# Kernel optimization log

Hardware: AMD Instinct MI355X
Metric: run time of the kernel (lower is better)

## Reference

```python
import jax, jax.numpy as jnp
import numpy as np

N_NODES = 50000


def gcn_conv(x, edge_index, W, b, n_nodes):
    # PyG GCNConv: add self-loops, symmetric normalization, linear, scatter-add.
    src, dst = edge_index[0], edge_index[1]
    loops = jnp.arange(n_nodes, dtype=src.dtype)
    src = jnp.concatenate([src, loops])
    dst = jnp.concatenate([dst, loops])
    # linear transform first (PyG order), reduces scatter width when out < in
    h = x @ W  # [N, out]
    deg = jax.ops.segment_sum(jnp.ones_like(dst, dtype=h.dtype), dst, num_segments=n_nodes)
    dinv = jnp.where(deg > 0, jax.lax.rsqrt(deg), 0.0)
    norm = dinv[src] * dinv[dst]  # [E+N]
    msgs = h[src] * norm[:, None]  # gather + scale, [E+N, out]
    out = jax.ops.segment_sum(msgs, dst, num_segments=n_nodes)  # scatter-add
    return out + b


def setup_inputs() -> dict:
    key = jax.random.key(0)
    k1, k2, k3, k4 = jax.random.split(key, 4)
    in_c, hid_c, out_c = 256, 128, 64
    n_edges = 800000
    features = jax.random.normal(k1, (N_NODES, in_c), dtype=jnp.float32)
    edge_index = jax.random.randint(k2, (2, n_edges), 0, N_NODES, dtype=jnp.int64)
    W1 = jax.random.normal(k3, (in_c, hid_c), dtype=jnp.float32) * (1.0 / np.sqrt(in_c))
    b1 = jnp.zeros((hid_c,), dtype=jnp.float32)
    W2 = jax.random.normal(k4, (hid_c, out_c), dtype=jnp.float32) * (1.0 / np.sqrt(hid_c))
    b2 = jnp.zeros((out_c,), dtype=jnp.float32)
    return {"features": features, "edge_index": edge_index, "W1": W1, "b1": b1, "W2": W2, "b2": b2}


def reference(features, edge_index, W1, b1, W2, b2):
    n = features.shape[0]
    x = gcn_conv(features, edge_index, W1, b1, n)
    x = jax.nn.relu(x)
    # dropout p=0.5 is identity at inference
    x = gcn_conv(x, edge_index, W2, b2, n)
    return x
```

## Files before the change

### kernel.cpp

```cpp
#include <hip/hip_runtime.h>

#define THREADS 256
#define SEG 64

typedef _Float16 f16;
typedef f16   f16x8 __attribute__((ext_vector_type(8)));
typedef float f32x4 __attribute__((ext_vector_type(4)));

__global__ void k_zero(unsigned* __restrict__ cnt, int n4){
  int i = blockIdx.x*blockDim.x + threadIdx.x;
  if(i < n4) ((int4*)cnt)[i] = make_int4(0,0,0,0);
}

template<int K, int N>
__global__ void k_build_gemm1(const int* __restrict__ ei, unsigned* __restrict__ cnt,
                              unsigned short* __restrict__ ssrc, int E, int M,
                              const float* __restrict__ A, const float* __restrict__ W,
                              f16* __restrict__ Hh, int buildBlocks){
  constexpr int BM = 64, BK = 32, BN = N;
  constexpr int AST = 40;
  constexpr int NM = 4, NN = 2;
  constexpr int SKN = BK*BN/THREADS;
  __shared__ f16 Ah[BM*AST], Bh[BN*AST];

  if((int)blockIdx.x < buildBlocks){
    const int grp = blockIdx.x & 7;
    const int nb  = blockIdx.x >> 3;
    const int lo  = grp * (M >> 3);
    const int hi  = (grp == 7) ? M : lo + (M >> 3);
    int e = nb*THREADS + threadIdx.x;
    if(e < E){
      int d = ei[E+e];
      if(d >= lo && d < hi){
        int s = ei[e];
        unsigned p = atomicAdd(&cnt[d], 1u);
        if(p < SEG) ssrc[(size_t)d*SEG + p] = (unsigned short)s;
      }
    }
    return;
  }

  const int bx   = (int)blockIdx.x - buildBlocks;
  const int tid  = threadIdx.x;
  const int row0 = bx*BM;
  const int wc = tid>>6, l = tid&63;
  const int lr = l&15, lk = l>>4;

  const int sar = tid>>2, sak = (tid&3)*8;
  const long long garow = min(row0+sar, M-1);
  const int sc = tid & (BN-1), sk0 = (tid>>7)*SKN;

  f32x4 acc[NM][NN] = {};

  for(int k0 = 0; k0 < K; k0 += BK){
    float avals[8];
    #pragma unroll
    for(int q=0;q<2;q++){
      float4 v = *(const float4*)(A + garow*K + k0 + sak + q*4);
      avals[q*4+0]=v.x; avals[q*4+1]=v.y; avals[q*4+2]=v.z; avals[q*4+3]=v.w;
    }
    float bvals[SKN];
    #pragma unroll
    for(int i=0;i<SKN;i++) bvals[i] = W[(size_t)(k0+sk0+i)*N + sc];

    __syncthreads();

    {
      f16x8 hv;
      #pragma unroll
      for(int j=0;j<8;j++) hv[j] = (f16)avals[j];
      *(f16x8*)&Ah[sar*AST + sak] = hv;
    }
    #pragma unroll
    for(int s=0;s<SKN/8;s++){
      f16x8 hv;
      #pragma unroll
      for(int j=0;j<8;j++) hv[j] = (f16)bvals[s*8+j];
      *(f16x8*)&Bh[sc*AST + sk0 + s*8] = hv;
    }
    __syncthreads();

    f16x8 af[NM], bf[NN];
    #pragma unroll
    for(int m=0;m<NM;m++){
      int r = m*16 + lr;
      af[m] = *(const f16x8*)&Ah[r*AST + lk*8];
    }
    #pragma unroll
    for(int n=0;n<NN;n++){
      int c = wc*32 + n*16 + lr;
      bf[n] = *(const f16x8*)&Bh[c*AST + lk*8];
    }
    #pragma unroll
    for(int m=0;m<NM;m++)
      #pragma unroll
      for(int n=0;n<NN;n++)
        acc[m][n] = __builtin_amdgcn_mfma_f32_16x16x32_f16(af[m], bf[n], acc[m][n], 0,0,0);
  }

  #pragma unroll
  for(int m=0;m<NM;m++){
    int grb = row0 + m*16 + lk*4;
    #pragma unroll
    for(int reg=0;reg<4;reg++){
      int gr = grb + reg;
      if(gr < M){
        #pragma unroll
        for(int n=0;n<NN;n++){
          int gc = wc*32 + n*16 + lr;
          Hh[(size_t)gr*N + gc] = (f16)(acc[m][n][reg]);
        }
      }
    }
  }
}

template<int K, int N>
__global__ void k_gemm_mfma_f16a(const f16* __restrict__ A, const float* __restrict__ W,
                                 const unsigned* __restrict__ cnt, f16* __restrict__ Hh, int M){
  constexpr int BM = 64, BK = 32, BN = N;
  constexpr int AST = 40;
  constexpr int NM = 4;
  constexpr int SKN = BK*BN/THREADS;
  __shared__ f16 Ah[BM*AST], Bh[BN*AST];

  const int tid  = threadIdx.x;
  const int row0 = blockIdx.x*BM;
  const int wc = tid>>6, l = tid&63;
  const int lr = l&15, lk = l>>4;

  const int sar = tid>>2, sak = (tid&3)*8;
  const long long garow = min(row0+sar, M-1);
  const int sc = tid & (BN-1), sk0 = (tid>>6)*SKN;

  f32x4 acc[NM] = {};

  for(int k0 = 0; k0 < K; k0 += BK){
    f16x8 av = *(const f16x8*)(A + garow*K + k0 + sak);
    float bvals[SKN];
    #pragma unroll
    for(int i=0;i<SKN;i++) bvals[i] = W[(size_t)(k0+sk0+i)*N + sc];

    __syncthreads();

    *(f16x8*)&Ah[sar*AST + sak] = av;
    {
      f16x8 hv;
      #pragma unroll
      for(int j=0;j<8;j++) hv[j] = (f16)bvals[j];
      *(f16x8*)&Bh[sc*AST + sk0] = hv;
    }
    __syncthreads();

    f16x8 af[NM], bf;
    #pragma unroll
    for(int m=0;m<NM;m++){
      int r = m*16 + lr;
      af[m] = *(const f16x8*)&Ah[r*AST + lk*8];
    }
    {
      int c = wc*16 + lr;
      bf = *(const f16x8*)&Bh[c*AST + lk*8];
    }
    #pragma unroll
    for(int m=0;m<NM;m++)
      acc[m] = __builtin_amdgcn_mfma_f32_16x16x32_f16(af[m], bf, acc[m], 0,0,0);
  }

  #pragma unroll
  for(int m=0;m<NM;m++){
    int grb = row0 + m*16 + lk*4;
    #pragma unroll
    for(int reg=0;reg<4;reg++){
      int gr = grb + reg;
      if(gr < M){
        float dv = rsqrtf((float)(cnt[gr] + 1u));
        int gc = wc*16 + lr;
        Hh[(size_t)gr*N + gc] = (f16)(acc[m][reg] * dv);
      }
    }
  }
}

__global__ void k_gather_l1(const unsigned* __restrict__ cnt,
                            const unsigned short* __restrict__ ssrc,
                            const f16* __restrict__ g,
                            const float* __restrict__ bias, f16* __restrict__ outh, int M){
  const int w = (blockIdx.x*blockDim.x + threadIdx.x) >> 6;
  const int l = threadIdx.x & 63;
  if(w >= M) return;
  const int q = l>>4, c = l&15;
  const f16x8* g8 = (const f16x8*)g;
  float acc[8] = {0.f,0.f,0.f,0.f,0.f,0.f,0.f,0.f};
  const int ne = min((int)cnt[w], SEG);
  int it = ne >> 2;
  int i = w*SEG + q;
  while(it >= 2){
    int s0 = (int)ssrc[i], s1 = (int)ssrc[i+4];
    float d0 = rsqrtf((float)(cnt[s0] + 1u));
    float d1 = rsqrtf((float)(cnt[s1] + 1u));
    f16x8 v0 = g8[(size_t)s0*16 + c];
    f16x8 v1 = g8[(size_t)s1*16 + c];
    #pragma unroll
    for(int j=0;j<8;j++){
      acc[j] = fmaf((float)v0[j], d0, acc[j]);
      acc[j] = fmaf((float)v1[j], d1, acc[j]);
    }
    i += 8; it -= 2;
  }
  if(it){
    int s = (int)ssrc[i];
    float ds = rsqrtf((float)(cnt[s] + 1u));
    f16x8 v = g8[(size_t)s*16 + c];
    #pragma unroll
    for(int j=0;j<8;j++) acc[j] = fmaf((float)v[j], ds, acc[j]);
    i += 4;
  }
  if(q < (ne & 3)){
    int s = (int)ssrc[i];
    float ds = rsqrtf((float)(cnt[s] + 1u));
    f16x8 v = g8[(size_t)s*16 + c];
    #pragma unroll
    for(int j=0;j<8;j++) acc[j] = fmaf((float)v[j], ds, acc[j]);
  }
  const float dw = rsqrtf((float)(cnt[w] + 1u));
  if(q == 0){
    f16x8 v = g8[(size_t)w*16 + c];
    #pragma unroll
    for(int j=0;j<8;j++) acc[j] = fmaf((float)v[j], dw, acc[j]);
  }
  #pragma unroll
  for(int j=0;j<8;j++){
    acc[j] += __shfl_xor(acc[j], 16);
    acc[j] += __shfl_xor(acc[j], 32);
  }
  if(q == 0){
    float4 b0 = ((const float4*)bias)[c*2];
    float4 b1 = ((const float4*)bias)[c*2+1];
    f16x8 o;
    o[0] = (f16)fmaxf(fmaf(acc[0], dw, b0.x), 0.f);
    o[1] = (f16)fmaxf(fmaf(acc[1], dw, b0.y), 0.f);
    o[2] = (f16)fmaxf(fmaf(acc[2], dw, b0.z), 0.f);
    o[3] = (f16)fmaxf(fmaf(acc[3], dw, b0.w), 0.f);
    o[4] = (f16)fmaxf(fmaf(acc[4], dw, b1.x), 0.f);
    o[5] = (f16)fmaxf(fmaf(acc[5], dw, b1.y), 0.f);
    o[6] = (f16)fmaxf(fmaf(acc[6], dw, b1.z), 0.f);
    o[7] = (f16)fmaxf(fmaf(acc[7], dw, b1.w), 0.f);
    ((f16x8*)outh)[(size_t)w*16 + c] = o;
  }
}

__global__ void k_gather_l2(const unsigned* __restrict__ cnt,
                            const unsigned short* __restrict__ ssrc,
                            const f16* __restrict__ g,
                            const float* __restrict__ bias, float* __restrict__ out, int M){
  const int w = (blockIdx.x*blockDim.x + threadIdx.x) >> 6;
  const int l = threadIdx.x & 63;
  if(w >= M) return;
  const int grp = l>>3, c = l&7;
  const f16x8* g8 = (const f16x8*)g;
  float acc[8] = {0.f,0.f,0.f,0.f,0.f,0.f,0.f,0.f};
  const int ne = min((int)cnt[w], SEG);
  int it = ne >> 3;
  int i = w*SEG + grp;
  while(it >= 2){
    int s0 = (int)ssrc[i], s1 = (int)ssrc[i+8];
    f16x8 v0 = g8[(size_t)s0*8 + c];
    f16x8 v1 = g8[(size_t)s1*8 + c];
    #pragma unroll
    for(int j=0;j<8;j++) acc[j] += (float)v0[j] + (float)v1[j];
    i += 16; it -= 2;
  }
  if(it){
    int s = (int)ssrc[i];
    f16x8 v = g8[(size_t)s*8 + c];
    #pragma unroll
    for(int j=0;j<8;j++) acc[j] += (float)v[j];
    i += 8;
  }
  if(grp < (ne & 7)){
    int s = (int)ssrc[i];
    f16x8 v = g8[(size_t)s*8 + c];
    #pragma unroll
    for(int j=0;j<8;j++) acc[j] += (float)v[j];
  }
  if(grp == 0){
    f16x8 v = g8[(size_t)w*8 + c];
    #pragma unroll
    for(int j=0;j<8;j++) acc[j] += (float)v[j];
  }
  #pragma unroll
  for(int j=0;j<8;j++){
    acc[j] += __shfl_xor(acc[j], 8);
    acc[j] += __shfl_xor(acc[j], 16);
    acc[j] += __shfl_xor(acc[j], 32);
  }
  if(grp == 0){
    const float dw = rsqrtf((float)(cnt[w] + 1u));
    float4 b0 = ((const float4*)bias)[c*2];
    float4 b1 = ((const float4*)bias)[c*2+1];
    float4 o0, o1;
    o0.x = fmaf(acc[0], dw, b0.x);
    o0.y = fmaf(acc[1], dw, b0.y);
    o0.z = fmaf(acc[2], dw, b0.z);
    o0.w = fmaf(acc[3], dw, b0.w);
    o1.x = fmaf(acc[4], dw, b1.x);
    o1.y = fmaf(acc[5], dw, b1.y);
    o1.z = fmaf(acc[6], dw, b1.z);
    o1.w = fmaf(acc[7], dw, b1.w);
    ((float4*)out)[(size_t)w*16 + c*2]     = o0;
    ((float4*)out)[(size_t)w*16 + c*2 + 1] = o1;
  }
}

extern "C" void kernel_launch(void* const* d_in, const int* in_sizes, int n_in,
                              void* d_out, int out_size, void* d_ws, size_t ws_size,
                              hipStream_t stream){
  const float* feat = (const float*)d_in[0];
  const int*   ei   = (const int*)d_in[1];
  const float* W1   = (const float*)d_in[2];
  const float* b1   = (const float*)d_in[3];
  const float* W2   = (const float*)d_in[4];
  const float* b2   = (const float*)d_in[5];
  float* out = (float*)d_out;

  const int M = in_sizes[0] / 256;
  const int E = in_sizes[1] / 2;

  float* ws = (float*)d_ws;
  unsigned*       cnt  = (unsigned*)ws;
  unsigned short* ssrc = (unsigned short*)(ws + 51200);
  f16*            h1h  = (f16*)(ws + 1651200);
  f16*            o1h  = (f16*)(ws + 4851200);
  f16*            h2h  = h1h;

  const int nbE = (E + THREADS-1)/THREADS;
  const int buildBlocks = nbE*8;
  const int gemmBlocks = (M + 63)/64;
  const int n4 = (M + 3)/4;

  k_zero<<<(n4 + THREADS-1)/THREADS, THREADS, 0, stream>>>(cnt, n4);

  k_build_gemm1<256,128><<<buildBlocks + gemmBlocks, THREADS, 0, stream>>>(
      ei, cnt, ssrc, E, M, feat, W1, h1h, buildBlocks);

  k_gather_l1<<<(M*64 + THREADS-1)/THREADS, THREADS, 0, stream>>>(cnt, ssrc, h1h, b1, o1h, M);

  k_gemm_mfma_f16a<128,64><<<gemmBlocks, THREADS, 0, stream>>>(o1h, W2, cnt, h2h, M);
  k_gather_l2<<<(M*64 + THREADS-1)/THREADS, THREADS, 0, stream>>>(cnt, ssrc, h2h, b2, out, M);
}
```

Baseline: 129.9 us.

## Split build from GEMM1 and fold source-degree scaling into GEMM1 epilogue

Separates the edge-list build from the first GEMM into its own kernel, so GEMM1 can read the finished degree counts and pre-scale each output row by its dinv. The layer-1 gather then sums plain rows and no longer loads cnt[src] or computes rsqrt per edge, applying only the destination scale at the end. Nontemporal loads are added for the edge index and the feature matrix. The cost is losing the overlap between the atomic-heavy build and the GEMM, which were fused into one launch before, plus one extra kernel launch.

```diff
diff --git a/kernel.cpp b/kernel.cpp
--- a/kernel.cpp
+++ b/kernel.cpp
@@ -6,43 +6,41 @@
 typedef _Float16 f16;
 typedef f16   f16x8 __attribute__((ext_vector_type(8)));
 typedef float f32x4 __attribute__((ext_vector_type(4)));
+typedef float fvec4 __attribute__((ext_vector_type(4)));
 
 __global__ void k_zero(unsigned* __restrict__ cnt, int n4){
   int i = blockIdx.x*blockDim.x + threadIdx.x;
   if(i < n4) ((int4*)cnt)[i] = make_int4(0,0,0,0);
 }
 
+__global__ void k_build(const int* __restrict__ ei, unsigned* __restrict__ cnt,
+                        unsigned short* __restrict__ ssrc, int E, int M){
+  const int grp = blockIdx.x & 7;
+  const int nb  = blockIdx.x >> 3;
+  const int lo  = grp * (M >> 3);
+  const int hi  = (grp == 7) ? M : lo + (M >> 3);
+  int e = nb*THREADS + threadIdx.x;
+  if(e < E){
+    int d = __builtin_nontemporal_load(ei + E + e);
+    if(d >= lo && d < hi){
+      int s = __builtin_nontemporal_load(ei + e);
+      unsigned p = atomicAdd(&cnt[d], 1u);
+      if(p < SEG) ssrc[(size_t)d*SEG + p] = (unsigned short)s;
+    }
+  }
+}
+
 template<int K, int N>
-__global__ void k_build_gemm1(const int* __restrict__ ei, unsigned* __restrict__ cnt,
-                              unsigned short* __restrict__ ssrc, int E, int M,
-                              const float* __restrict__ A, const float* __restrict__ W,
-                              f16* __restrict__ Hh, int buildBlocks){
+__global__ void k_gemm1(const float* __restrict__ A, const float* __restrict__ W,
+                        const unsigned* __restrict__ cnt, f16* __restrict__ Hh, int M){
   constexpr int BM = 64, BK = 32, BN = N;
   constexpr int AST = 40;
   constexpr int NM = 4, NN = 2;
   constexpr int SKN = BK*BN/THREADS;
   __shared__ f16 Ah[BM*AST], Bh[BN*AST];
 
-  if((int)blockIdx.x < buildBlocks){
-    const int grp = blockIdx.x & 7;
-    const int nb  = blockIdx.x >> 3;
-    const int lo  = grp * (M >> 3);
-    const int hi  = (grp == 7) ? M : lo + (M >> 3);
-    int e = nb*THREADS + threadIdx.x;
-    if(e < E){
-      int d = ei[E+e];
-      if(d >= lo && d < hi){
-        int s = ei[e];
-        unsigned p = atomicAdd(&cnt[d], 1u);
-        if(p < SEG) ssrc[(size_t)d*SEG + p] = (unsigned short)s;
-      }
-    }
-    return;
-  }
-
-  const int bx   = (int)blockIdx.x - buildBlocks;
   const int tid  = threadIdx.x;
-  const int row0 = bx*BM;
+  const int row0 = blockIdx.x*BM;
   const int wc = tid>>6, l = tid&63;
   const int lr = l&15, lk = l>>4;
 
@@ -56,7 +54,7 @@
     float avals[8];
     #pragma unroll
     for(int q=0;q<2;q++){
-      float4 v = *(const float4*)(A + garow*K + k0 + sak + q*4);
+      fvec4 v = __builtin_nontemporal_load((const fvec4*)(A + garow*K + k0 + sak + q*4));
       avals[q*4+0]=v.x; avals[q*4+1]=v.y; avals[q*4+2]=v.z; avals[q*4+3]=v.w;
     }
     float bvals[SKN];
@@ -105,10 +103,11 @@
     for(int reg=0;reg<4;reg++){
       int gr = grb + reg;
       if(gr < M){
+        float dv = rsqrtf((float)(cnt[gr] + 1u));
         #pragma unroll
         for(int n=0;n<NN;n++){
           int gc = wc*32 + n*16 + lr;
-          Hh[(size_t)gr*N + gc] = (f16)(acc[m][n][reg]);
+          Hh[(size_t)gr*N + gc] = (f16)(acc[m][n][reg] * dv);
         }
       }
     }
@@ -197,37 +196,29 @@
   int i = w*SEG + q;
   while(it >= 2){
     int s0 = (int)ssrc[i], s1 = (int)ssrc[i+4];
-    float d0 = rsqrtf((float)(cnt[s0] + 1u));
-    float d1 = rsqrtf((float)(cnt[s1] + 1u));
     f16x8 v0 = g8[(size_t)s0*16 + c];
     f16x8 v1 = g8[(size_t)s1*16 + c];
     #pragma unroll
-    for(int j=0;j<8;j++){
-      acc[j] = fmaf((float)v0[j], d0, acc[j]);
-      acc[j] = fmaf((float)v1[j], d1, acc[j]);
-    }
+    for(int j=0;j<8;j++) acc[j] += (float)v0[j] + (float)v1[j];
     i += 8; it -= 2;
   }
   if(it){
     int s = (int)ssrc[i];
-    float ds = rsqrtf((float)(cnt[s] + 1u));
     f16x8 v = g8[(size_t)s*16 + c];
     #pragma unroll
-    for(int j=0;j<8;j++) acc[j] = fmaf((float)v[j], ds, acc[j]);
+    for(int j=0;j<8;j++) acc[j] += (float)v[j];
     i += 4;
   }
   if(q < (ne & 3)){
     int s = (int)ssrc[i];
-    float ds = rsqrtf((float)(cnt[s] + 1u));
     f16x8 v = g8[(size_t)s*16 + c];
     #pragma unroll
-    for(int j=0;j<8;j++) acc[j] = fmaf((float)v[j], ds, acc[j]);
-  }
-  const float dw = rsqrtf((float)(cnt[w] + 1u));
+    for(int j=0;j<8;j++) acc[j] += (float)v[j];
+  }
   if(q == 0){
     f16x8 v = g8[(size_t)w*16 + c];
     #pragma unroll
-    for(int j=0;j<8;j++) acc[j] = fmaf((float)v[j], dw, acc[j]);
+    for(int j=0;j<8;j++) acc[j] += (float)v[j];
   }
   #pragma unroll
   for(int j=0;j<8;j++){
@@ -235,6 +226,7 @@
     acc[j] += __shfl_xor(acc[j], 32);
   }
   if(q == 0){
+    const float dw = rsqrtf((float)(cnt[w] + 1u));
     float4 b0 = ((const float4*)bias)[c*2];
     float4 b1 = ((const float4*)bias)[c*2+1];
     f16x8 o;
@@ -335,15 +327,13 @@
   f16*            h2h  = h1h;
 
   const int nbE = (E + THREADS-1)/THREADS;
-  const int buildBlocks = nbE*8;
   const int gemmBlocks = (M + 63)/64;
   const int n4 = (M + 3)/4;
 
   k_zero<<<(n4 + THREADS-1)/THREADS, THREADS, 0, stream>>>(cnt, n4);
-
-  k_build_gemm1<256,128><<<buildBlocks + gemmBlocks, THREADS, 0, stream>>>(
-      ei, cnt, ssrc, E, M, feat, W1, h1h, buildBlocks);
-
+  k_build<<<nbE*8, THREADS, 0, stream>>>(ei, cnt, ssrc, E, M);
+
+  k_gemm1<256,128><<<gemmBlocks, THREADS, 0, stream>>>(feat, W1, cnt, h1h, M);
   k_gather_l1<<<(M*64 + THREADS-1)/THREADS, THREADS, 0, stream>>>(cnt, ssrc, h1h, b1, o1h, M);
 
   k_gemm_mfma_f16a<128,64><<<gemmBlocks, THREADS, 0, stream>>>(o1h, W2, cnt, h2h, M);
```

Measured after the change: 142.1 us. 1.09x slower.
